# Kernel tuning notes

Measured on AMD Instinct MI355X. Metric: run time of the kernel, lower is better.

## Reference

```python
import jax, jax.numpy as jnp
import numpy as np

NUM_EXPERTS = 8
TOP_K = 2
BALANCE_LOSS_COEF = 0.01


def setup_inputs() -> dict:
    key = jax.random.key(0)
    ks = jax.random.split(key, 5)
    B, S, H, I, E = 8, 2048, 512, 2048, NUM_EXPERTS
    return {
        "hidden_states": jax.random.normal(ks[0], (B, S, H), dtype=jnp.float32),
        "Wg": jax.random.normal(ks[1], (H, E), dtype=jnp.float32) * (1.0 / np.sqrt(H)),
        "bg": jnp.zeros((E,), dtype=jnp.float32),
        "W1": jax.random.normal(ks[2], (E, H, I), dtype=jnp.float32) * (1.0 / np.sqrt(H)),
        "b1": jnp.zeros((E, I), dtype=jnp.float32),
        "W2": jax.random.normal(ks[3], (E, I, H), dtype=jnp.float32) * (1.0 / np.sqrt(I)),
        "b2": jnp.zeros((E, H), dtype=jnp.float32),
    }


def reference(hidden_states, Wg, bg, W1, b1, W2, b2):
    B, S, H = hidden_states.shape
    E, K = NUM_EXPERTS, TOP_K

    # ---- Router: softmax gate + top-k, renormalized weights ----
    logits = jnp.einsum('bsh,he->bse', hidden_states, Wg) + bg       # [B,S,E]
    probs = jax.nn.softmax(logits, axis=-1)                          # [B,S,E]
    top_p, top_i = jax.lax.top_k(probs, K)                           # [B,S,K]
    routing_weights = top_p / jnp.sum(top_p, axis=-1, keepdims=True)  # [B,S,K]

    # ---- Experts: compute every expert densely (small fixed E), then gather ----
    h = jnp.einsum('bsh,ehi->ebsi', hidden_states, W1) + b1[:, None, None, :]
    h = jax.nn.gelu(h)
    y = jnp.einsum('ebsi,eih->ebsh', h, W2) + b2[:, None, None, :]   # [E,B,S,H]

    y = jnp.moveaxis(y, 0, 2)                                        # [B,S,E,H]
    sel = jnp.take_along_axis(y, top_i[..., None], axis=2)           # [B,S,K,H]
    output = jnp.sum(routing_weights[..., None] * sel, axis=2) + hidden_states

    # ---- Load balancing loss (Switch-style): E * sum_e f_e * P_e ----
    assign = jnp.sum(jax.nn.one_hot(top_i, E, dtype=probs.dtype), axis=2)  # [B,S,E]
    f = jnp.mean(assign, axis=(0, 1)) / K                            # fraction dispatched
    P = jnp.mean(probs, axis=(0, 1))                                 # mean router prob
    balance_loss = BALANCE_LOSS_COEF * E * jnp.sum(f * P)

    return output, balance_loss
```

## Files before the change

kernel.cpp:

```cpp
#include <hip/hip_runtime.h>

#define BS_TOK 16384
#define HD 512
#define IDIM 2048
#define NE 8
#define RT_MAX 264
#define CAP (RT_MAX * 128)

typedef unsigned short u16;
typedef unsigned int u32;
typedef __attribute__((ext_vector_type(8))) __bf16 bf16x8;
typedef __attribute__((ext_vector_type(4))) float f32x4;

__device__ __forceinline__ u16 f2bf(float f) {
  u32 u = __builtin_bit_cast(u32, f);
  u += 0x7fffu + ((u >> 16) & 1u);
  return (u16)(u >> 16);
}
__device__ __forceinline__ u16 f2bf_hw(float f) {
  u32 r;
  asm("v_cvt_pk_bf16_f32 %0, %1, %2" : "=v"(r) : "v"(f), "v"(f));
  return (u16)r;
}
__device__ __forceinline__ float bflo(u32 u) { return __builtin_bit_cast(float, u << 16); }
__device__ __forceinline__ float bfhi(u32 u) { return __builtin_bit_cast(float, u & 0xffff0000u); }
__device__ __forceinline__ float gelu_t(float v) {
  float t = v * (-2.302558f - 0.1029474f * v * v);
  return v * __builtin_amdgcn_rcpf(1.0f + __builtin_amdgcn_exp2f(t));
}
__device__ __forceinline__ void gload16(const u16* g, u16* l) {
  __builtin_amdgcn_global_load_lds((const __attribute__((address_space(1))) u16*)g,
                                   (__attribute__((address_space(3))) u16*)l, 16, 0, 0);
}

__global__ void k_transpose2(const float* __restrict__ W1, u16* __restrict__ W1T,
                             const float* __restrict__ W2, u16* __restrict__ W2T) {
  __shared__ float t[32][33];
  int z = blockIdx.z;
  const float* in; u16* out; int R, C, bx, by;
  if (z < NE) { in = W1; out = W1T; R = HD; C = IDIM; bx = blockIdx.x; by = blockIdx.y; }
  else { in = W2; out = W2T; R = IDIM; C = HD; bx = blockIdx.y; by = blockIdx.x; z -= NE; }
  size_t eb = (size_t)z * HD * IDIM;
  int c0 = bx * 32, r0 = by * 32;
  int tx = threadIdx.x, ty = threadIdx.y;
  #pragma unroll
  for (int j = ty; j < 32; j += 8) t[j][tx] = in[eb + (size_t)(r0 + j) * C + (c0 + tx)];
  __syncthreads();
  #pragma unroll
  for (int j = ty; j < 32; j += 8) out[eb + (size_t)(c0 + j) * R + (r0 + tx)] = f2bf_hw(t[tx][j]);
}

__global__ void k_router(const float* __restrict__ x, const float* __restrict__ Wg,
                         const float* __restrict__ bg, int* __restrict__ top_e,
                         float* __restrict__ top_w, u32* __restrict__ counts,
                         float* __restrict__ Psum, u16* __restrict__ xb) {
  __shared__ float wg_s[HD * NE];
  __shared__ float Pp[NE];
  __shared__ u32 cnt[NE];
  int tid = threadIdx.x;
  if (tid < NE) { Pp[tid] = 0.f; cnt[tid] = 0; }
  for (int i = tid; i < HD * NE; i += 256) wg_s[i] = Wg[i];
  __syncthreads();
  int wv = tid >> 6, lane = tid & 63;
  int t = blockIdx.x * 4 + wv;
  const float4* xr = (const float4*)(x + (size_t)t * HD + lane * 8);
  float4 a = xr[0], b = xr[1];
  u32 p0 = f2bf(a.x) | ((u32)f2bf(a.y) << 16);
  u32 p1 = f2bf(a.z) | ((u32)f2bf(a.w) << 16);
  u32 p2 = f2bf(b.x) | ((u32)f2bf(b.y) << 16);
  u32 p3 = f2bf(b.z) | ((u32)f2bf(b.w) << 16);
  ((uint4*)(xb + (size_t)t * HD))[lane] = make_uint4(p0, p1, p2, p3);

  float acc[NE];
  #pragma unroll
  for (int e = 0; e < NE; ++e) acc[e] = 0.f;
  #pragma unroll
  for (int j = 0; j < 8; ++j) {
    float xv = j < 4 ? (&a.x)[j] : (&b.x)[j - 4];
    int h = lane * 8 + j;
    #pragma unroll
    for (int e = 0; e < NE; ++e) acc[e] += xv * wg_s[h * NE + e];
  }
  #pragma unroll
  for (int off = 32; off > 0; off >>= 1) {
    #pragma unroll
    for (int e = 0; e < NE; ++e) acc[e] += __shfl_down(acc[e], off);
  }
  if (lane == 0) {
    float lg[NE];
    #pragma unroll
    for (int e = 0; e < NE; ++e) lg[e] = acc[e] + bg[e];
    int i1 = 0; float m1 = lg[0];
    #pragma unroll
    for (int e = 1; e < NE; ++e) if (lg[e] > m1) { m1 = lg[e]; i1 = e; }
    int i2 = -1; float m2 = -1e30f;
    #pragma unroll
    for (int e = 0; e < NE; ++e) if (e != i1 && lg[e] > m2) { m2 = lg[e]; i2 = e; }
    float s = 0.f, p[NE];
    #pragma unroll
    for (int e = 0; e < NE; ++e) { p[e] = __expf(lg[e] - m1); s += p[e]; }
    float inv = 1.f / s;
    #pragma unroll
    for (int e = 0; e < NE; ++e) { p[e] *= inv; atomicAdd(&Pp[e], p[e]); }
    float denom = p[i1] + p[i2];
    top_e[2 * t] = i1; top_e[2 * t + 1] = i2;
    top_w[2 * t] = p[i1] / denom; top_w[2 * t + 1] = p[i2] / denom;
    atomicAdd(&cnt[i1], 1u); atomicAdd(&cnt[i2], 1u);
  }
  __syncthreads();
  if (tid < NE) { atomicAdd(&counts[tid], cnt[tid]); atomicAdd(&Psum[tid], Pp[tid]); }
}

__global__ void k_scan(const u32* __restrict__ counts, const float* __restrict__ Psum,
                       u32* __restrict__ padoff, u32* __restrict__ pos, float* __restrict__ out) {
  if (threadIdx.x == 0) {
    u32 off = 0; float loss = 0.f;
    for (int e = 0; e < NE; ++e) {
      padoff[e] = off; pos[e] = off;
      off += ((counts[e] + 127u) / 128u) * 128u;
      loss += ((float)counts[e] / (float)(BS_TOK * 2)) * (Psum[e] / (float)BS_TOK);
    }
    padoff[NE] = off;
    out[(size_t)BS_TOK * HD] = 0.01f * (float)NE * loss;
  }
}

__global__ void k_scatter(const int* __restrict__ top_e, const float* __restrict__ top_w,
                          u32* __restrict__ pos, int* __restrict__ perm_t,
                          float* __restrict__ perm_w, int* __restrict__ inv) {
  int g = blockIdx.x * 256 + threadIdx.x;
  int e = top_e[g]; float wgt = top_w[g];
  int lane = threadIdx.x & 63;
  #pragma unroll
  for (int ee = 0; ee < NE; ++ee) {
    unsigned long long m = __ballot(e == ee);
    if (e == ee) {
      int nb = __popcll(m & ((1ull << lane) - 1ull));
      int leader = __ffsll((unsigned long long)m) - 1;
      u32 base = 0;
      if (lane == leader) base = atomicAdd(&pos[ee], (u32)__popcll(m));
      base = __shfl(base, leader);
      int slot = (int)base + nb;
      perm_t[slot] = g >> 1;
      perm_w[slot] = wgt;
      inv[g] = slot;
    }
  }
}

__global__ void k_outinit(const float* __restrict__ x, float* __restrict__ out) {
  size_t i = (size_t)blockIdx.x * 256 + threadIdx.x;
  ((float4*)out)[i] = ((const float4*)x)[i];
}

template <int KSTEPS, int NCT, int NTOT, bool GATHER, bool ACT, bool ATOMIC>
__global__ __launch_bounds__(256, 2) void k_gemm(
    const u16* __restrict__ A, int lda, const u16* __restrict__ W,
    const float* __restrict__ bias, const int* __restrict__ perm_t,
    const float* __restrict__ perm_w, const u32* __restrict__ padoff,
    u16* __restrict__ C, float* __restrict__ outA, int rt0) {
  __shared__ u16 As[2][8192], Bs[2][8192];
  int nb = gridDim.x;
  int b = blockIdx.x;
  int tile = (b & 7) * (nb >> 3) + (b >> 3);
  int rt = rt0 + tile / NCT, ct = tile % NCT;
  u32 s0 = (u32)rt * 128u;
  if (rt >= RT_MAX || s0 >= padoff[NE]) return;
  int e = 0;
  #pragma unroll
  for (int k = 1; k < NE; ++k) e += (s0 >= padoff[k]) ? 1 : 0;

  int tid = threadIdx.x;
  int wv = tid >> 6, lane = tid & 63;
  int l15 = lane & 15, lg4 = lane >> 4;
  int wr = wv >> 1, wc = wv & 1;

  int srow = tid >> 3;
  int cb = (tid & 7) * 16;
  int cbs = (cb ^ ((srow & 7) << 4)) >> 1;

  const u16* ap[4]; const u16* bp[4];
  #pragma unroll
  for (int i = 0; i < 4; ++i) {
    int r = i * 32 + srow;
    int arow = GATHER ? perm_t[s0 + r] : (int)(s0 + r);
    ap[i] = A + (size_t)arow * lda + cbs;
    bp[i] = W + ((size_t)e * NTOT + ct * 128 + r) * (KSTEPS * 64) + cbs;
  }

  int base_n = ct * 128 + wc * 64;
  f32x4 acc[4][4];
  #pragma unroll
  for (int j = 0; j < 4; ++j) {
    float bv = bias[e * NTOT + base_n + j * 16 + l15];
    #pragma unroll
    for (int i = 0; i < 4; ++i) acc[i][j] = f32x4{bv, bv, bv, bv};
  }

  #pragma unroll
  for (int i = 0; i < 4; ++i) gload16(ap[i], As[0] + tid * 8 + i * 2048);
  #pragma unroll
  for (int i = 0; i < 4; ++i) gload16(bp[i], Bs[0] + tid * 8 + i * 2048);
  #pragma unroll
  for (int i = 0; i < 4; ++i) gload16(ap[i] + 64, As[1] + tid * 8 + i * 2048);
  #pragma unroll
  for (int i = 0; i < 4; ++i) gload16(bp[i] + 64, Bs[1] + tid * 8 + i * 2048);
  asm volatile("s_waitcnt vmcnt(8)" ::: "memory");
  __builtin_amdgcn_sched_barrier(0);
  __builtin_amdgcn_s_barrier();

  for (int ks = 0; ks < KSTEPS; ++ks) {
    int cur = ks & 1;
    const u16* Ab = As[cur];
    const u16* Bb = Bs[cur];
    bf16x8 af[2][4], bf[2][4];
    #pragma unroll
    for (int kk = 0; kk < 2; ++kk) {
      #pragma unroll
      for (int f = 0; f < 4; ++f) {
        int ra = wr * 64 + f * 16 + l15;
        af[kk][f] = *(const bf16x8*)((const char*)Ab +
                    (ra * 128 + ((kk * 64 + lg4 * 16) ^ ((ra & 7) << 4))));
        int rb = wc * 64 + f * 16 + l15;
        bf[kk][f] = *(const bf16x8*)((const char*)Bb +
                    (rb * 128 + ((kk * 64 + lg4 * 16) ^ ((rb & 7) << 4))));
      }
    }
    asm volatile("s_waitcnt lgkmcnt(0)" ::: "memory");
    __builtin_amdgcn_sched_barrier(0);
    __builtin_amdgcn_s_barrier();

    if (ks + 2 < KSTEPS) {
      int k0 = (ks + 2) * 64;
      #pragma unroll
      for (int i = 0; i < 4; ++i) gload16(ap[i] + k0, As[cur] + tid * 8 + i * 2048);
      #pragma unroll
      for (int i = 0; i < 4; ++i) gload16(bp[i] + k0, Bs[cur] + tid * 8 + i * 2048);
    }

    __builtin_amdgcn_s_setprio(1);
    #pragma unroll
    for (int kk = 0; kk < 2; ++kk) {
      #pragma unroll
      for (int i = 0; i < 4; ++i)
        #pragma unroll
        for (int j = 0; j < 4; ++j)
          acc[i][j] = __builtin_amdgcn_mfma_f32_16x16x32_bf16(af[kk][i], bf[kk][j], acc[i][j], 0, 0, 0);
    }
    __builtin_amdgcn_s_setprio(0);

    if (ks + 1 < KSTEPS) {
      if (ks + 2 < KSTEPS) {
        asm volatile("s_waitcnt vmcnt(8)" ::: "memory");
      } else {
        asm volatile("s_waitcnt vmcnt(0)" ::: "memory");
      }
      __builtin_amdgcn_sched_barrier(0);
      __builtin_amdgcn_s_barrier();
    }
  }

  #pragma unroll
  for (int i = 0; i < 4; ++i) {
    u32 mrow = s0 + wr * 64 + i * 16 + lg4 * 4;
    #pragma unroll
    for (int rr = 0; rr < 4; ++rr) {
      u32 m = mrow + rr;
      if (ATOMIC) {
        int tok = perm_t[m]; float wt = perm_w[m];
        if (wt != 0.f) {
          #pragma unroll
          for (int j = 0; j < 4; ++j) {
            float v = acc[i][j][rr] * wt;
            atomicAdd(outA + (size_t)tok * HD + base_n + j * 16 + l15, v);
          }
        }
      } else {
        #pragma unroll
        for (int j = 0; j < 4; ++j) {
          float v = acc[i][j][rr];
          if (ACT) v = gelu_t(v);
          C[(size_t)m * NTOT + base_n + j * 16 + l15] = f2bf_hw(v);
        }
      }
    }
  }
}

__global__ void k_final(const float* __restrict__ x, const u16* __restrict__ y,
                        const int* __restrict__ inv, const float* __restrict__ top_w,
                        float* __restrict__ out) {
  int tid = threadIdx.x;
  int t = blockIdx.x * 4 + (tid >> 6);
  int lane = tid & 63;
  int s0 = inv[2 * t], s1 = inv[2 * t + 1];
  float w0 = top_w[2 * t], w1 = top_w[2 * t + 1];
  size_t xo = (size_t)t * HD + lane * 8;
  float4 a = *(const float4*)(x + xo);
  float4 b = *(const float4*)(x + xo + 4);
  uint4 ya = *(const uint4*)(y + (size_t)s0 * HD + lane * 8);
  uint4 yb = *(const uint4*)(y + (size_t)s1 * HD + lane * 8);
  float4 o0, o1;
  o0.x = a.x + w0 * bflo(ya.x) + w1 * bflo(yb.x);
  o0.y = a.y + w0 * bfhi(ya.x) + w1 * bfhi(yb.x);
  o0.z = a.z + w0 * bflo(ya.y) + w1 * bflo(yb.y);
  o0.w = a.w + w0 * bfhi(ya.y) + w1 * bfhi(yb.y);
  o1.x = b.x + w0 * bflo(ya.z) + w1 * bflo(yb.z);
  o1.y = b.y + w0 * bfhi(ya.z) + w1 * bfhi(yb.z);
  o1.z = b.z + w0 * bflo(ya.w) + w1 * bflo(yb.w);
  o1.w = b.w + w0 * bfhi(ya.w) + w1 * bfhi(yb.w);
  *(float4*)(out + xo) = o0;
  *(float4*)(out + xo + 4) = o1;
}

extern "C" void kernel_launch(void* const* d_in, const int* in_sizes, int n_in,
                              void* d_out, int out_size, void* d_ws, size_t ws_size,
                              hipStream_t stream) {
  const float* x  = (const float*)d_in[0];
  const float* Wg = (const float*)d_in[1];
  const float* bg = (const float*)d_in[2];
  const float* W1 = (const float*)d_in[3];
  const float* b1 = (const float*)d_in[4];
  const float* W2 = (const float*)d_in[5];
  const float* b2 = (const float*)d_in[6];
  float* out = (float*)d_out;

  char* w = (char*)d_ws;
  u32* counts  = (u32*)(w + 0);
  u32* pos     = (u32*)(w + 32);
  float* Psum  = (float*)(w + 64);
  u32* padoff  = (u32*)(w + 96);
  int* top_e   = (int*)(w + 256);
  float* top_w = (float*)(w + 256 + 131072);
  int* invm    = (int*)(w + 256 + 2 * 131072);
  int* perm_t  = (int*)(w + 256 + 3 * 131072);
  float* perm_w = (float*)(w + 256 + 3 * 131072 + 135168);
  u16* xb  = (u16*)(w + 663808);
  u16* W1T = (u16*)(w + 17441024);
  u16* W2T = (u16*)(w + 34218240);
  u16* h   = (u16*)(w + 50995456);
  u16* y   = (u16*)(w + 189407488);

  bool modeA = ws_size >= 224010496ull;
  int T;
  if (modeA) {
    T = RT_MAX;
  } else {
    size_t hspace = ws_size > 50995456ull ? ws_size - 50995456ull : 0;
    T = (int)(hspace / (128ull * IDIM * 2));
    T &= ~1;
    if (T < 2) return;
    if (T > RT_MAX) T = RT_MAX;
  }

  (void)hipMemsetAsync(w, 0, 256, stream);
  (void)hipMemsetAsync(w + 393472, 0, 270336, stream);
  k_transpose2<<<dim3(IDIM / 32, HD / 32, 2 * NE), dim3(32, 8), 0, stream>>>(W1, W1T, W2, W2T);
  k_router<<<BS_TOK / 4, 256, 0, stream>>>(x, Wg, bg, top_e, top_w, counts, Psum, xb);
  k_scan<<<1, 64, 0, stream>>>(counts, Psum, padoff, pos, out);
  k_scatter<<<(BS_TOK * 2) / 256, 256, 0, stream>>>(top_e, top_w, pos, perm_t, perm_w, invm);
  if (!modeA) k_outinit<<<(BS_TOK * HD / 4) / 256, 256, 0, stream>>>(x, out);

  int nch = (RT_MAX + T - 1) / T;
  for (int c = 0; c < nch; ++c) {
    int rt0 = c * T;
    u16* hadj = h - (size_t)rt0 * 128 * IDIM;
    k_gemm<8, 16, IDIM, true, true, false><<<T * 16, 256, 0, stream>>>(
        xb, HD, W1T, b1, perm_t, perm_w, padoff, hadj, nullptr, rt0);
    if (modeA) {
      k_gemm<32, 4, HD, false, false, false><<<T * 4, 256, 0, stream>>>(
          hadj, IDIM, W2T, b2, perm_t, perm_w, padoff, y, nullptr, rt0);
    } else {
      k_gemm<32, 4, HD, false, false, true><<<T * 4, 256, 0, stream>>>(
          hadj, IDIM, W2T, b2, perm_t, perm_w, padoff, nullptr, out, rt0);
    }
  }
  if (modeA) k_final<<<BS_TOK / 4, 256, 0, stream>>>(x, y, invm, top_w, out);
}
```

Measured before the change: 364.7 us.

## Use 256x256 tiles for expert GEMM1, fuse scan into scatter, atomic-combine GEMM2

```diff
diff --git a/kernel.cpp b/kernel.cpp
--- a/kernel.cpp
+++ b/kernel.cpp
@@ -4,8 +4,9 @@
 #define HD 512
 #define IDIM 2048
 #define NE 8
-#define RT_MAX 264
-#define CAP (RT_MAX * 128)
+#define RT256 136
+#define RT128 272
+#define CAP (RT256 * 256)
 
 typedef unsigned short u16;
 typedef unsigned int u32;
@@ -23,7 +24,6 @@
   return (u16)r;
 }
 __device__ __forceinline__ float bflo(u32 u) { return __builtin_bit_cast(float, u << 16); }
-__device__ __forceinline__ float bfhi(u32 u) { return __builtin_bit_cast(float, u & 0xffff0000u); }
 __device__ __forceinline__ float gelu_t(float v) {
   float t = v * (-2.302558f - 0.1029474f * v * v);
   return v * __builtin_amdgcn_rcpf(1.0f + __builtin_amdgcn_exp2f(t));
@@ -111,23 +111,26 @@
   if (tid < NE) { atomicAdd(&counts[tid], cnt[tid]); atomicAdd(&Psum[tid], Pp[tid]); }
 }
 
-__global__ void k_scan(const u32* __restrict__ counts, const float* __restrict__ Psum,
-                       u32* __restrict__ padoff, u32* __restrict__ pos, float* __restrict__ out) {
+__global__ void k_scatter(const int* __restrict__ top_e, const float* __restrict__ top_w,
+                          const u32* __restrict__ counts, const float* __restrict__ Psum,
+                          u32* __restrict__ pos_rel, int* __restrict__ perm_t,
+                          float* __restrict__ perm_w, u32* __restrict__ padoff,
+                          float* __restrict__ out) {
+  __shared__ u32 po[NE];
   if (threadIdx.x == 0) {
     u32 off = 0; float loss = 0.f;
     for (int e = 0; e < NE; ++e) {
-      padoff[e] = off; pos[e] = off;
-      off += ((counts[e] + 127u) / 128u) * 128u;
+      po[e] = off;
+      off += ((counts[e] + 255u) / 256u) * 256u;
       loss += ((float)counts[e] / (float)(BS_TOK * 2)) * (Psum[e] / (float)BS_TOK);
     }
-    padoff[NE] = off;
-    out[(size_t)BS_TOK * HD] = 0.01f * (float)NE * loss;
-  }
-}
-
-__global__ void k_scatter(const int* __restrict__ top_e, const float* __restrict__ top_w,
-                          u32* __restrict__ pos, int* __restrict__ perm_t,
-                          float* __restrict__ perm_w, int* __restrict__ inv) {
+    if (blockIdx.x == 0) {
+      for (int e = 0; e < NE; ++e) padoff[e] = po[e];
+      padoff[NE] = off;
+      out[(size_t)BS_TOK * HD] = 0.01f * (float)NE * loss;
+    }
+  }
+  __syncthreads();
   int g = blockIdx.x * 256 + threadIdx.x;
   int e = top_e[g]; float wgt = top_w[g];
   int lane = threadIdx.x & 63;
@@ -138,12 +141,11 @@
       int nb = __popcll(m & ((1ull << lane) - 1ull));
       int leader = __ffsll((unsigned long long)m) - 1;
       u32 base = 0;
-      if (lane == leader) base = atomicAdd(&pos[ee], (u32)__popcll(m));
+      if (lane == leader) base = atomicAdd(&pos_rel[ee], (u32)__popcll(m));
       base = __shfl(base, leader);
-      int slot = (int)base + nb;
+      int slot = (int)(po[ee] + base) + nb;
       perm_t[slot] = g >> 1;
       perm_w[slot] = wgt;
-      inv[g] = slot;
     }
   }
 }
@@ -153,19 +155,136 @@
   ((float4*)out)[i] = ((const float4*)x)[i];
 }
 
-template <int KSTEPS, int NCT, int NTOT, bool GATHER, bool ACT, bool ATOMIC>
-__global__ __launch_bounds__(256, 2) void k_gemm(
-    const u16* __restrict__ A, int lda, const u16* __restrict__ W,
-    const float* __restrict__ bias, const int* __restrict__ perm_t,
+__global__ __launch_bounds__(512, 2) void k_gemm1(
+    const u16* __restrict__ xb, const u16* __restrict__ W1T,
+    const float* __restrict__ b1, const int* __restrict__ perm_t,
+    const u32* __restrict__ padoff, u16* __restrict__ h) {
+  __shared__ u16 As[2][16384], Bs[2][16384];
+  int nb = gridDim.x;
+  int b = blockIdx.x;
+  int tile = (b & 7) * (nb >> 3) + (b >> 3);
+  int rt = tile >> 3, ct = tile & 7;
+  u32 s0 = (u32)rt * 256u;
+  if (s0 >= padoff[NE]) return;
+  int e = 0;
+  #pragma unroll
+  for (int k = 1; k < NE; ++k) e += (s0 >= padoff[k]) ? 1 : 0;
+
+  int tid = threadIdx.x;
+  int wv = tid >> 6, lane = tid & 63;
+  int l15 = lane & 15, lg4 = lane >> 4;
+  int wm = wv >> 2, wn = wv & 3;
+
+  int cb = (tid & 7) * 16;
+  const u16* ap[4]; const u16* bp[4];
+  #pragma unroll
+  for (int i = 0; i < 4; ++i) {
+    int row = (tid >> 3) + i * 64;
+    int off = (cb ^ ((row & 7) << 4)) >> 1;
+    ap[i] = xb + (size_t)perm_t[s0 + row] * HD + off;
+    bp[i] = W1T + ((size_t)e * IDIM + ct * 256 + row) * HD + off;
+  }
+
+  int base_n = ct * 256 + wn * 64;
+  f32x4 acc[8][4];
+  #pragma unroll
+  for (int fc = 0; fc < 4; ++fc) {
+    float bv = b1[(size_t)e * IDIM + base_n + fc * 16 + l15];
+    #pragma unroll
+    for (int fr = 0; fr < 8; ++fr) acc[fr][fc] = f32x4{bv, bv, bv, bv};
+  }
+
+  #pragma unroll
+  for (int i = 0; i < 4; ++i) gload16(ap[i], As[0] + tid * 8 + i * 4096);
+  #pragma unroll
+  for (int i = 0; i < 4; ++i) gload16(bp[i], Bs[0] + tid * 8 + i * 4096);
+  #pragma unroll
+  for (int i = 0; i < 4; ++i) gload16(ap[i] + 64, As[1] + tid * 8 + i * 4096);
+  #pragma unroll
+  for (int i = 0; i < 4; ++i) gload16(bp[i] + 64, Bs[1] + tid * 8 + i * 4096);
+  asm volatile("s_waitcnt vmcnt(8)" ::: "memory");
+  __builtin_amdgcn_sched_barrier(0);
+  __builtin_amdgcn_s_barrier();
+
+  for (int ks = 0; ks < 8; ++ks) {
+    int cur = ks & 1;
+    const u16* Ab = As[cur];
+    const u16* Bb = Bs[cur];
+    bf16x8 af[2][8], bf[2][4];
+    #pragma unroll
+    for (int kk = 0; kk < 2; ++kk) {
+      #pragma unroll
+      for (int fr = 0; fr < 8; ++fr) {
+        int ra = wm * 128 + fr * 16 + l15;
+        af[kk][fr] = *(const bf16x8*)((const char*)Ab +
+                     (ra * 128 + ((kk * 64 + lg4 * 16) ^ ((ra & 7) << 4))));
+      }
+      #pragma unroll
+      for (int fc = 0; fc < 4; ++fc) {
+        int rb = wn * 64 + fc * 16 + l15;
+        bf[kk][fc] = *(const bf16x8*)((const char*)Bb +
+                     (rb * 128 + ((kk * 64 + lg4 * 16) ^ ((rb & 7) << 4))));
+      }
+    }
+    asm volatile("s_waitcnt lgkmcnt(0)" ::: "memory");
+    __builtin_amdgcn_sched_barrier(0);
+    __builtin_amdgcn_s_barrier();
+
+    if (ks + 2 < 8) {
+      int k0 = (ks + 2) * 64;
+      #pragma unroll
+      for (int i = 0; i < 4; ++i) gload16(ap[i] + k0, As[cur] + tid * 8 + i * 4096);
+      #pragma unroll
+      for (int i = 0; i < 4; ++i) gload16(bp[i] + k0, Bs[cur] + tid * 8 + i * 4096);
+    }
+
+    __builtin_amdgcn_s_setprio(1);
+    #pragma unroll
+    for (int kk = 0; kk < 2; ++kk)
+      #pragma unroll
+      for (int fr = 0; fr < 8; ++fr)
+        #pragma unroll
+        for (int fc = 0; fc < 4; ++fc)
+          acc[fr][fc] = __builtin_amdgcn_mfma_f32_16x16x32_bf16(af[kk][fr], bf[kk][fc], acc[fr][fc], 0, 0, 0);
+    __builtin_amdgcn_s_setprio(0);
+
+    if (ks + 1 < 8) {
+      if (ks + 2 < 8) {
+        asm volatile("s_waitcnt vmcnt(8)" ::: "memory");
+      } else {
+        asm volatile("s_waitcnt vmcnt(0)" ::: "memory");
+      }
+      __builtin_amdgcn_sched_barrier(0);
+      __builtin_amdgcn_s_barrier();
+    }
+  }
+
+  #pragma unroll
+  for (int fr = 0; fr < 8; ++fr) {
+    u32 mrow = s0 + wm * 128 + fr * 16 + lg4 * 4;
+    #pragma unroll
+    for (int rr = 0; rr < 4; ++rr) {
+      #pragma unroll
+      for (int fc = 0; fc < 4; ++fc) {
+        float v = gelu_t(acc[fr][fc][rr]);
+        h[(size_t)(mrow + rr) * IDIM + base_n + fc * 16 + l15] = f2bf_hw(v);
+      }
+    }
+  }
+}
+
+__global__ __launch_bounds__(256, 2) void k_gemm2(
+    const u16* __restrict__ h, const u16* __restrict__ W2T,
+    const float* __restrict__ b2, const int* __restrict__ perm_t,
     const float* __restrict__ perm_w, const u32* __restrict__ padoff,
-    u16* __restrict__ C, float* __restrict__ outA, int rt0) {
+    float* __restrict__ out) {
   __shared__ u16 As[2][8192], Bs[2][8192];
   int nb = gridDim.x;
   int b = blockIdx.x;
   int tile = (b & 7) * (nb >> 3) + (b >> 3);
-  int rt = rt0 + tile / NCT, ct = tile % NCT;
+  int rt = tile >> 2, ct = tile & 3;
   u32 s0 = (u32)rt * 128u;
-  if (rt >= RT_MAX || s0 >= padoff[NE]) return;
+  if (s0 >= padoff[NE]) return;
   int e = 0;
   #pragma unroll
   for (int k = 1; k < NE; ++k) e += (s0 >= padoff[k]) ? 1 : 0;
@@ -183,16 +302,15 @@
   #pragma unroll
   for (int i = 0; i < 4; ++i) {
     int r = i * 32 + srow;
-    int arow = GATHER ? perm_t[s0 + r] : (int)(s0 + r);
-    ap[i] = A + (size_t)arow * lda + cbs;
-    bp[i] = W + ((size_t)e * NTOT + ct * 128 + r) * (KSTEPS * 64) + cbs;
+    ap[i] = h + (size_t)(s0 + r) * IDIM + cbs;
+    bp[i] = W2T + ((size_t)e * HD + ct * 128 + r) * IDIM + cbs;
   }
 
   int base_n = ct * 128 + wc * 64;
   f32x4 acc[4][4];
   #pragma unroll
   for (int j = 0; j < 4; ++j) {
-    float bv = bias[e * NTOT + base_n + j * 16 + l15];
+    float bv = b2[e * HD + base_n + j * 16 + l15];
     #pragma unroll
     for (int i = 0; i < 4; ++i) acc[i][j] = f32x4{bv, bv, bv, bv};
   }
@@ -209,7 +327,7 @@
   __builtin_amdgcn_sched_barrier(0);
   __builtin_amdgcn_s_barrier();
 
-  for (int ks = 0; ks < KSTEPS; ++ks) {
+  for (int ks = 0; ks < 32; ++ks) {
     int cur = ks & 1;
     const u16* Ab = As[cur];
     const u16* Bb = Bs[cur];
@@ -230,7 +348,7 @@
     __builtin_amdgcn_sched_barrier(0);
     __builtin_amdgcn_s_barrier();
 
-    if (ks + 2 < KSTEPS) {
+    if (ks + 2 < 32) {
       int k0 = (ks + 2) * 64;
       #pragma unroll
       for (int i = 0; i < 4; ++i) gload16(ap[i] + k0, As[cur] + tid * 8 + i * 2048);
@@ -240,17 +358,16 @@
 
     __builtin_amdgcn_s_setprio(1);
     #pragma unroll
-    for (int kk = 0; kk < 2; ++kk) {
+    for (int kk = 0; kk < 2; ++kk)
       #pragma unroll
       for (int i = 0; i < 4; ++i)
         #pragma unroll
         for (int j = 0; j < 4; ++j)
           acc[i][j] = __builtin_amdgcn_mfma_f32_16x16x32_bf16(af[kk][i], bf[kk][j], acc[i][j], 0, 0, 0);
-    }
     __builtin_amdgcn_s_setprio(0);
 
-    if (ks + 1 < KSTEPS) {
-      if (ks + 2 < KSTEPS) {
+    if (ks + 1 < 32) {
+      if (ks + 2 < 32) {
         asm volatile("s_waitcnt vmcnt(8)" ::: "memory");
       } else {
         asm volatile("s_waitcnt vmcnt(0)" ::: "memory");
@@ -266,51 +383,16 @@
     #pragma unroll
     for (int rr = 0; rr < 4; ++rr) {
       u32 m = mrow + rr;
-      if (ATOMIC) {
-        int tok = perm_t[m]; float wt = perm_w[m];
-        if (wt != 0.f) {
-          #pragma unroll
-          for (int j = 0; j < 4; ++j) {
-            float v = acc[i][j][rr] * wt;
-            atomicAdd(outA + (size_t)tok * HD + base_n + j * 16 + l15, v);
-          }
-        }
-      } else {
+      int tok = perm_t[m]; float wt = perm_w[m];
+      if (wt != 0.f) {
         #pragma unroll
         for (int j = 0; j < 4; ++j) {
-          float v = acc[i][j][rr];
-          if (ACT) v = gelu_t(v);
-          C[(size_t)m * NTOT + base_n + j * 16 + l15] = f2bf_hw(v);
+          float v = acc[i][j][rr] * wt;
+          atomicAdd(out + (size_t)tok * HD + base_n + j * 16 + l15, v);
         }
       }
     }
   }
-}
-
-__global__ void k_final(const float* __restrict__ x, const u16* __restrict__ y,
-                        const int* __restrict__ inv, const float* __restrict__ top_w,
-                        float* __restrict__ out) {
-  int tid = threadIdx.x;
-  int t = blockIdx.x * 4 + (tid >> 6);
-  int lane = tid & 63;
-  int s0 = inv[2 * t], s1 = inv[2 * t + 1];
-  float w0 = top_w[2 * t], w1 = top_w[2 * t + 1];
-  size_t xo = (size_t)t * HD + lane * 8;
-  float4 a = *(const float4*)(x + xo);
-  float4 b = *(const float4*)(x + xo + 4);
-  uint4 ya = *(const uint4*)(y + (size_t)s0 * HD + lane * 8);
-  uint4 yb = *(const uint4*)(y + (size_t)s1 * HD + lane * 8);
-  float4 o0, o1;
-  o0.x = a.x + w0 * bflo(ya.x) + w1 * bflo(yb.x);
-  o0.y = a.y + w0 * bfhi(ya.x) + w1 * bfhi(yb.x);
-  o0.z = a.z + w0 * bflo(ya.y) + w1 * bflo(yb.y);
-  o0.w = a.w + w0 * bfhi(ya.y) + w1 * bfhi(yb.y);
-  o1.x = b.x + w0 * bflo(ya.z) + w1 * bflo(yb.z);
-  o1.y = b.y + w0 * bfhi(ya.z) + w1 * bfhi(yb.z);
-  o1.z = b.z + w0 * bflo(ya.w) + w1 * bflo(yb.w);
-  o1.w = b.w + w0 * bfhi(ya.w) + w1 * bfhi(yb.w);
-  *(float4*)(out + xo) = o0;
-  *(float4*)(out + xo + 4) = o1;
 }
 
 extern "C" void kernel_launch(void* const* d_in, const int* in_sizes, int n_in,
@@ -326,54 +408,26 @@
   float* out = (float*)d_out;
 
   char* w = (char*)d_ws;
-  u32* counts  = (u32*)(w + 0);
-  u32* pos     = (u32*)(w + 32);
-  float* Psum  = (float*)(w + 64);
-  u32* padoff  = (u32*)(w + 96);
-  int* top_e   = (int*)(w + 256);
-  float* top_w = (float*)(w + 256 + 131072);
-  int* invm    = (int*)(w + 256 + 2 * 131072);
-  int* perm_t  = (int*)(w + 256 + 3 * 131072);
-  float* perm_w = (float*)(w + 256 + 3 * 131072 + 135168);
-  u16* xb  = (u16*)(w + 663808);
-  u16* W1T = (u16*)(w + 17441024);
-  u16* W2T = (u16*)(w + 34218240);
-  u16* h   = (u16*)(w + 50995456);
-  u16* y   = (u16*)(w + 189407488);
-
-  bool modeA = ws_size >= 224010496ull;
-  int T;
-  if (modeA) {
-    T = RT_MAX;
-  } else {
-    size_t hspace = ws_size > 50995456ull ? ws_size - 50995456ull : 0;
-    T = (int)(hspace / (128ull * IDIM * 2));
-    T &= ~1;
-    if (T < 2) return;
-    if (T > RT_MAX) T = RT_MAX;
-  }
-
-  (void)hipMemsetAsync(w, 0, 256, stream);
-  (void)hipMemsetAsync(w + 393472, 0, 270336, stream);
+  u32* counts   = (u32*)(w + 0);
+  u32* pos_rel  = (u32*)(w + 32);
+  float* Psum   = (float*)(w + 64);
+  u32* padoff   = (u32*)(w + 96);
+  int* top_e    = (int*)(w + 256);
+  float* top_w  = (float*)(w + 131328);
+  int* perm_t   = (int*)(w + 262400);
+  float* perm_w = (float*)(w + 401664);
+  u16* xb  = (u16*)(w + 540928);
+  u16* W1T = (u16*)(w + 17318144);
+  u16* W2T = (u16*)(w + 34095360);
+  u16* h   = (u16*)(w + 50872576);
+  if (ws_size < 193478912ull) return;
+
+  (void)hipMemsetAsync(w, 0, 540928, stream);
+  k_outinit<<<(BS_TOK * HD / 4) / 256, 256, 0, stream>>>(x, out);
   k_transpose2<<<dim3(IDIM / 32, HD / 32, 2 * NE), dim3(32, 8), 0, stream>>>(W1, W1T, W2, W2T);
   k_router<<<BS_TOK / 4, 256, 0, stream>>>(x, Wg, bg, top_e, top_w, counts, Psum, xb);
-  k_scan<<<1, 64, 0, stream>>>(counts, Psum, padoff, pos, out);
-  k_scatter<<<(BS_TOK * 2) / 256, 256, 0, stream>>>(top_e, top_w, pos, perm_t, perm_w, invm);
-  if (!modeA) k_outinit<<<(BS_TOK * HD / 4) / 256, 256, 0, stream>>>(x, out);
-
-  int nch = (RT_MAX + T - 1) / T;
-  for (int c = 0; c < nch; ++c) {
-    int rt0 = c * T;
-    u16* hadj = h - (size_t)rt0 * 128 * IDIM;
-    k_gemm<8, 16, IDIM, true, true, false><<<T * 16, 256, 0, stream>>>(
-        xb, HD, W1T, b1, perm_t, perm_w, padoff, hadj, nullptr, rt0);
-    if (modeA) {
-      k_gemm<32, 4, HD, false, false, false><<<T * 4, 256, 0, stream>>>(
-          hadj, IDIM, W2T, b2, perm_t, perm_w, padoff, y, nullptr, rt0);
-    } else {
-      k_gemm<32, 4, HD, false, false, true><<<T * 4, 256, 0, stream>>>(
-          hadj, IDIM, W2T, b2, perm_t, perm_w, padoff, nullptr, out, rt0);
-    }
-  }
-  if (modeA) k_final<<<BS_TOK / 4, 256, 0, stream>>>(x, y, invm, top_w, out);
-}
+  k_scatter<<<(BS_TOK * 2) / 256, 256, 0, stream>>>(top_e, top_w, counts, Psum,
+                                                    pos_rel, perm_t, perm_w, padoff, out);
+  k_gemm1<<<RT256 * 8, 512, 0, stream>>>(xb, W1T, b1, perm_t, padoff, h);
+  k_gemm2<<<RT128 * 4, 256, 0, stream>>>(h, W2T, b2, perm_t, perm_w, padoff, out);
+}
```

Result: slower. 429.0 us (+17.6%).

## Merge transpose and router, fold scan into scatter, drop chunked fallback

Applied to the files above, without the earlier changes.

```diff
diff --git a/kernel.cpp b/kernel.cpp
--- a/kernel.cpp
+++ b/kernel.cpp
@@ -33,36 +33,39 @@
                                    (__attribute__((address_space(3))) u16*)l, 16, 0, 0);
 }
 
-__global__ void k_transpose2(const float* __restrict__ W1, u16* __restrict__ W1T,
-                             const float* __restrict__ W2, u16* __restrict__ W2T) {
-  __shared__ float t[32][33];
-  int z = blockIdx.z;
-  const float* in; u16* out; int R, C, bx, by;
-  if (z < NE) { in = W1; out = W1T; R = HD; C = IDIM; bx = blockIdx.x; by = blockIdx.y; }
-  else { in = W2; out = W2T; R = IDIM; C = HD; bx = blockIdx.y; by = blockIdx.x; z -= NE; }
-  size_t eb = (size_t)z * HD * IDIM;
-  int c0 = bx * 32, r0 = by * 32;
-  int tx = threadIdx.x, ty = threadIdx.y;
-  #pragma unroll
-  for (int j = ty; j < 32; j += 8) t[j][tx] = in[eb + (size_t)(r0 + j) * C + (c0 + tx)];
-  __syncthreads();
-  #pragma unroll
-  for (int j = ty; j < 32; j += 8) out[eb + (size_t)(c0 + j) * R + (r0 + tx)] = f2bf_hw(t[tx][j]);
-}
-
-__global__ void k_router(const float* __restrict__ x, const float* __restrict__ Wg,
-                         const float* __restrict__ bg, int* __restrict__ top_e,
-                         float* __restrict__ top_w, u32* __restrict__ counts,
-                         float* __restrict__ Psum, u16* __restrict__ xb) {
+__global__ void k_prep(const float* __restrict__ W1, u16* __restrict__ W1T,
+                       const float* __restrict__ W2, u16* __restrict__ W2T,
+                       const float* __restrict__ x, const float* __restrict__ Wg,
+                       const float* __restrict__ bg, int* __restrict__ top_e,
+                       float* __restrict__ top_w, u32* __restrict__ counts,
+                       float* __restrict__ Psum, u16* __restrict__ xb) {
+  int bid = blockIdx.x;
+  int tid = threadIdx.x;
+  if (bid < 16384) {
+    __shared__ float t[32][33];
+    int z = bid >> 10, rem = bid & 1023;
+    int gy = rem >> 6, gx = rem & 63;
+    const float* in; u16* out; int R, C, bx, by;
+    if (z < NE) { in = W1; out = W1T; R = HD; C = IDIM; bx = gx; by = gy; }
+    else { in = W2; out = W2T; R = IDIM; C = HD; bx = gy; by = gx; z -= NE; }
+    size_t eb = (size_t)z * HD * IDIM;
+    int c0 = bx * 32, r0 = by * 32;
+    int tx = tid & 31, ty = tid >> 5;
+    #pragma unroll
+    for (int j = ty; j < 32; j += 8) t[j][tx] = in[eb + (size_t)(r0 + j) * C + (c0 + tx)];
+    __syncthreads();
+    #pragma unroll
+    for (int j = ty; j < 32; j += 8) out[eb + (size_t)(c0 + j) * R + (r0 + tx)] = f2bf_hw(t[tx][j]);
+    return;
+  }
   __shared__ float wg_s[HD * NE];
   __shared__ float Pp[NE];
   __shared__ u32 cnt[NE];
-  int tid = threadIdx.x;
   if (tid < NE) { Pp[tid] = 0.f; cnt[tid] = 0; }
   for (int i = tid; i < HD * NE; i += 256) wg_s[i] = Wg[i];
   __syncthreads();
   int wv = tid >> 6, lane = tid & 63;
-  int t = blockIdx.x * 4 + wv;
+  int t = (bid - 16384) * 4 + wv;
   const float4* xr = (const float4*)(x + (size_t)t * HD + lane * 8);
   float4 a = xr[0], b = xr[1];
   u32 p0 = f2bf(a.x) | ((u32)f2bf(a.y) << 16);
@@ -77,9 +80,9 @@
   #pragma unroll
   for (int j = 0; j < 8; ++j) {
     float xv = j < 4 ? (&a.x)[j] : (&b.x)[j - 4];
-    int h = lane * 8 + j;
-    #pragma unroll
-    for (int e = 0; e < NE; ++e) acc[e] += xv * wg_s[h * NE + e];
+    int hh = lane * 8 + j;
+    #pragma unroll
+    for (int e = 0; e < NE; ++e) acc[e] += xv * wg_s[hh * NE + e];
   }
   #pragma unroll
   for (int off = 32; off > 0; off >>= 1) {
@@ -111,23 +114,26 @@
   if (tid < NE) { atomicAdd(&counts[tid], cnt[tid]); atomicAdd(&Psum[tid], Pp[tid]); }
 }
 
-__global__ void k_scan(const u32* __restrict__ counts, const float* __restrict__ Psum,
-                       u32* __restrict__ padoff, u32* __restrict__ pos, float* __restrict__ out) {
+__global__ void k_scatter(const int* __restrict__ top_e, const float* __restrict__ top_w,
+                          const u32* __restrict__ counts, const float* __restrict__ Psum,
+                          u32* __restrict__ pos_rel, int* __restrict__ perm_t,
+                          float* __restrict__ perm_w, u32* __restrict__ padoff,
+                          int* __restrict__ inv, float* __restrict__ out) {
+  __shared__ u32 po[NE];
   if (threadIdx.x == 0) {
     u32 off = 0; float loss = 0.f;
     for (int e = 0; e < NE; ++e) {
-      padoff[e] = off; pos[e] = off;
+      po[e] = off;
       off += ((counts[e] + 127u) / 128u) * 128u;
       loss += ((float)counts[e] / (float)(BS_TOK * 2)) * (Psum[e] / (float)BS_TOK);
     }
-    padoff[NE] = off;
-    out[(size_t)BS_TOK * HD] = 0.01f * (float)NE * loss;
-  }
-}
-
-__global__ void k_scatter(const int* __restrict__ top_e, const float* __restrict__ top_w,
-                          u32* __restrict__ pos, int* __restrict__ perm_t,
-                          float* __restrict__ perm_w, int* __restrict__ inv) {
+    if (blockIdx.x == 0) {
+      for (int e = 0; e < NE; ++e) padoff[e] = po[e];
+      padoff[NE] = off;
+      out[(size_t)BS_TOK * HD] = 0.01f * (float)NE * loss;
+    }
+  }
+  __syncthreads();
   int g = blockIdx.x * 256 + threadIdx.x;
   int e = top_e[g]; float wgt = top_w[g];
   int lane = threadIdx.x & 63;
@@ -138,9 +144,9 @@
       int nb = __popcll(m & ((1ull << lane) - 1ull));
       int leader = __ffsll((unsigned long long)m) - 1;
       u32 base = 0;
-      if (lane == leader) base = atomicAdd(&pos[ee], (u32)__popcll(m));
+      if (lane == leader) base = atomicAdd(&pos_rel[ee], (u32)__popcll(m));
       base = __shfl(base, leader);
-      int slot = (int)base + nb;
+      int slot = (int)(po[ee] + base) + nb;
       perm_t[slot] = g >> 1;
       perm_w[slot] = wgt;
       inv[g] = slot;
@@ -148,24 +154,18 @@
   }
 }
 
-__global__ void k_outinit(const float* __restrict__ x, float* __restrict__ out) {
-  size_t i = (size_t)blockIdx.x * 256 + threadIdx.x;
-  ((float4*)out)[i] = ((const float4*)x)[i];
-}
-
-template <int KSTEPS, int NCT, int NTOT, bool GATHER, bool ACT, bool ATOMIC>
+template <int KSTEPS, int NCT, int NTOT, bool GATHER, bool ACT>
 __global__ __launch_bounds__(256, 2) void k_gemm(
     const u16* __restrict__ A, int lda, const u16* __restrict__ W,
     const float* __restrict__ bias, const int* __restrict__ perm_t,
-    const float* __restrict__ perm_w, const u32* __restrict__ padoff,
-    u16* __restrict__ C, float* __restrict__ outA, int rt0) {
+    const u32* __restrict__ padoff, u16* __restrict__ C) {
   __shared__ u16 As[2][8192], Bs[2][8192];
   int nb = gridDim.x;
   int b = blockIdx.x;
   int tile = (b & 7) * (nb >> 3) + (b >> 3);
-  int rt = rt0 + tile / NCT, ct = tile % NCT;
+  int rt = tile / NCT, ct = tile % NCT;
   u32 s0 = (u32)rt * 128u;
-  if (rt >= RT_MAX || s0 >= padoff[NE]) return;
+  if (s0 >= padoff[NE]) return;
   int e = 0;
   #pragma unroll
   for (int k = 1; k < NE; ++k) e += (s0 >= padoff[k]) ? 1 : 0;
@@ -240,13 +240,12 @@
 
     __builtin_amdgcn_s_setprio(1);
     #pragma unroll
-    for (int kk = 0; kk < 2; ++kk) {
+    for (int kk = 0; kk < 2; ++kk)
       #pragma unroll
       for (int i = 0; i < 4; ++i)
         #pragma unroll
         for (int j = 0; j < 4; ++j)
           acc[i][j] = __builtin_amdgcn_mfma_f32_16x16x32_bf16(af[kk][i], bf[kk][j], acc[i][j], 0, 0, 0);
-    }
     __builtin_amdgcn_s_setprio(0);
 
     if (ks + 1 < KSTEPS) {
@@ -266,22 +265,11 @@
     #pragma unroll
     for (int rr = 0; rr < 4; ++rr) {
       u32 m = mrow + rr;
-      if (ATOMIC) {
-        int tok = perm_t[m]; float wt = perm_w[m];
-        if (wt != 0.f) {
-          #pragma unroll
-          for (int j = 0; j < 4; ++j) {
-            float v = acc[i][j][rr] * wt;
-            atomicAdd(outA + (size_t)tok * HD + base_n + j * 16 + l15, v);
-          }
-        }
-      } else {
-        #pragma unroll
-        for (int j = 0; j < 4; ++j) {
-          float v = acc[i][j][rr];
-          if (ACT) v = gelu_t(v);
-          C[(size_t)m * NTOT + base_n + j * 16 + l15] = f2bf_hw(v);
-        }
+      #pragma unroll
+      for (int j = 0; j < 4; ++j) {
+        float v = acc[i][j][rr];
+        if (ACT) v = gelu_t(v);
+        C[(size_t)m * NTOT + base_n + j * 16 + l15] = f2bf_hw(v);
       }
     }
   }
@@ -326,54 +314,31 @@
   float* out = (float*)d_out;
 
   char* w = (char*)d_ws;
-  u32* counts  = (u32*)(w + 0);
-  u32* pos     = (u32*)(w + 32);
-  float* Psum  = (float*)(w + 64);
-  u32* padoff  = (u32*)(w + 96);
-  int* top_e   = (int*)(w + 256);
-  float* top_w = (float*)(w + 256 + 131072);
-  int* invm    = (int*)(w + 256 + 2 * 131072);
-  int* perm_t  = (int*)(w + 256 + 3 * 131072);
+  u32* counts   = (u32*)(w + 0);
+  u32* pos_rel  = (u32*)(w + 32);
+  float* Psum   = (float*)(w + 64);
+  u32* padoff   = (u32*)(w + 96);
+  int* top_e    = (int*)(w + 256);
+  float* top_w  = (float*)(w + 256 + 131072);
+  int* invm     = (int*)(w + 256 + 2 * 131072);
+  int* perm_t   = (int*)(w + 256 + 3 * 131072);
   float* perm_w = (float*)(w + 256 + 3 * 131072 + 135168);
   u16* xb  = (u16*)(w + 663808);
   u16* W1T = (u16*)(w + 17441024);
   u16* W2T = (u16*)(w + 34218240);
   u16* h   = (u16*)(w + 50995456);
   u16* y   = (u16*)(w + 189407488);
-
-  bool modeA = ws_size >= 224010496ull;
-  int T;
-  if (modeA) {
-    T = RT_MAX;
-  } else {
-    size_t hspace = ws_size > 50995456ull ? ws_size - 50995456ull : 0;
-    T = (int)(hspace / (128ull * IDIM * 2));
-    T &= ~1;
-    if (T < 2) return;
-    if (T > RT_MAX) T = RT_MAX;
-  }
-
-  (void)hipMemsetAsync(w, 0, 256, stream);
-  (void)hipMemsetAsync(w + 393472, 0, 270336, stream);
-  k_transpose2<<<dim3(IDIM / 32, HD / 32, 2 * NE), dim3(32, 8), 0, stream>>>(W1, W1T, W2, W2T);
-  k_router<<<BS_TOK / 4, 256, 0, stream>>>(x, Wg, bg, top_e, top_w, counts, Psum, xb);
-  k_scan<<<1, 64, 0, stream>>>(counts, Psum, padoff, pos, out);
-  k_scatter<<<(BS_TOK * 2) / 256, 256, 0, stream>>>(top_e, top_w, pos, perm_t, perm_w, invm);
-  if (!modeA) k_outinit<<<(BS_TOK * HD / 4) / 256, 256, 0, stream>>>(x, out);
-
-  int nch = (RT_MAX + T - 1) / T;
-  for (int c = 0; c < nch; ++c) {
-    int rt0 = c * T;
-    u16* hadj = h - (size_t)rt0 * 128 * IDIM;
-    k_gemm<8, 16, IDIM, true, true, false><<<T * 16, 256, 0, stream>>>(
-        xb, HD, W1T, b1, perm_t, perm_w, padoff, hadj, nullptr, rt0);
-    if (modeA) {
-      k_gemm<32, 4, HD, false, false, false><<<T * 4, 256, 0, stream>>>(
-          hadj, IDIM, W2T, b2, perm_t, perm_w, padoff, y, nullptr, rt0);
-    } else {
-      k_gemm<32, 4, HD, false, false, true><<<T * 4, 256, 0, stream>>>(
-          hadj, IDIM, W2T, b2, perm_t, perm_w, padoff, nullptr, out, rt0);
-    }
-  }
-  if (modeA) k_final<<<BS_TOK / 4, 256, 0, stream>>>(x, y, invm, top_w, out);
-}
+  if (ws_size < 224010496ull) return;
+
+  (void)hipMemsetAsync(w, 0, 663808, stream);
+  k_prep<<<20480, 256, 0, stream>>>(W1, W1T, W2, W2T, x, Wg, bg,
+                                    top_e, top_w, counts, Psum, xb);
+  k_scatter<<<(BS_TOK * 2) / 256, 256, 0, stream>>>(top_e, top_w, counts, Psum,
+                                                    pos_rel, perm_t, perm_w, padoff,
+                                                    invm, out);
+  k_gemm<8, 16, IDIM, true, true><<<RT_MAX * 16, 256, 0, stream>>>(
+      xb, HD, W1T, b1, perm_t, padoff, h);
+  k_gemm<32, 4, HD, false, false><<<RT_MAX * 4, 256, 0, stream>>>(
+      h, IDIM, W2T, b2, perm_t, padoff, y);
+  k_final<<<BS_TOK / 4, 256, 0, stream>>>(x, y, invm, top_w, out);
+}
```

New measurement: 359.0 us. Within noise of the previous version (-1.6%).
